# Kernel tuning notes

Measured on AMD Instinct MI355X. Metric: run time of the kernel, lower is better.

## Reference

```python
import jax, jax.numpy as jnp
import numpy as np

B, C, D, H, W = 2, 32, 16, 64, 64
SCALER = 8
CK = C // SCALER  # qk channels = 4


def setup_inputs() -> dict:
    key = jax.random.key(0)
    ks = jax.random.split(key, 8)
    s = 0.05
    return {
        "x": jax.random.normal(ks[0], (B, C, D, H, W), dtype=jnp.float32),
        "Wk": jax.random.normal(ks[1], (CK, C), dtype=jnp.float32) * s,
        "bk": jax.random.normal(ks[2], (CK,), dtype=jnp.float32) * s,
        "Wq": jax.random.normal(ks[3], (CK, C), dtype=jnp.float32) * s,
        "bq": jax.random.normal(ks[4], (CK,), dtype=jnp.float32) * s,
        "Wv": jax.random.normal(ks[5], (C, C), dtype=jnp.float32) * s,
        "bv": jax.random.normal(ks[6], (C,), dtype=jnp.float32) * s,
        "gamma": jnp.ones((1,), dtype=jnp.float32),
    }


def _proj(x, Wt, b):
    # 1x1x1 Conv3d == channel matmul: (o,c) x (b,c,d,h,w) -> (b,o,d,h,w)
    y = jnp.einsum('oc,bcdhw->bodhw', Wt, x) + b[None, :, None, None, None]
    return y


def reference(x, Wk, bk, Wq, bq, Wv, bv, gamma):
    b, c, d, h, w = x.shape
    hw = h * w
    xk = _proj(x, Wk, bk).reshape(b, -1, hw)   # (b, ck*d, hw)
    xq = _proj(x, Wq, bq).reshape(b, -1, hw)   # (b, ck*d, hw)
    xv = _proj(x, Wv, bv).reshape(b, -1, hw)   # (b, c*d,  hw)
    # dot[b,i,j] = sum_e xk[b,e,i] * xq[b,e,j]  -> (b, hw, hw)
    dot = jnp.einsum('bei,bej->bij', xk, xq)
    att = jax.nn.softmax(dot, axis=-1)          # softmax over last dim
    # x_a[b,m,i] = sum_j xv[b,m,j] * att[b,i,j]
    x_a = jnp.einsum('bmj,bij->bmi', xv, att)
    x_a = x_a.reshape(b, c, d, h, w)
    return gamma[0] * x + x_a
```

## Files before the change

kernel.cpp:

```cpp
#include <hip/hip_runtime.h>
#include <hip/hip_bf16.h>

#define B_   2
#define C_   32
#define D_   16
#define HW_  4096
#define CK_  4
#define E_   64
#define M_   512
#define JC_  4

typedef __attribute__((ext_vector_type(8)))  short bf16x8;
typedef __attribute__((ext_vector_type(16))) float f32x16;

union U4 { unsigned int u[4]; bf16x8 v; };

__device__ __forceinline__ short f2bf(float f) {
    __hip_bfloat16 h = __float2bfloat16(f);
    return *reinterpret_cast<short*>(&h);
}
__device__ __forceinline__ unsigned short f2bfu(float f) {
    __hip_bfloat16 h = __float2bfloat16(f);
    return *reinterpret_cast<unsigned short*>(&h);
}

__global__ void prep_kernel(
    const float* __restrict__ Wk, const float* __restrict__ bk,
    const float* __restrict__ Wq, const float* __restrict__ bq,
    const float* __restrict__ Wv, const float* __restrict__ bv,
    short* __restrict__ Wall, float* __restrict__ ball)
{
    int t = threadIdx.x;
    for (int i = t; i < 64*C_; i += 256) {
        int o = i >> 5, cc = i & 31;
        float val = (o < 32) ? Wv[o*C_ + cc]
                  : (o < 36) ? Wk[(o-32)*C_ + cc]
                  : (o < 40) ? Wq[(o-36)*C_ + cc] : 0.f;
        Wall[o*C_ + cc] = f2bf(val);
    }
    if (t < 64)
        ball[t] = (t < 32) ? bv[t] : (t < 36) ? bk[t-32] : (t < 40) ? bq[t-36] : 0.f;
}

__global__ __launch_bounds__(256) void proj_kernel(
    const float* __restrict__ x,
    const short* __restrict__ Wall, const float* __restrict__ ball,
    short* __restrict__ xk, short* __restrict__ xq,
    __hip_bfloat16* __restrict__ v)
{
    __shared__ short s_k[32*16], s_q[32*16];
    const int t    = threadIdx.x;
    const int lane = t & 63;
    const int w    = t >> 6;
    const int h    = lane >> 5;
    const int c    = lane & 31;

    const int pt = blockIdx.x & 127;
    const int dg = (blockIdx.x >> 7) & 3;
    const int b  = blockIdx.x >> 9;
    const int d  = dg*4 + w;
    const int p0 = pt*32;

    bf16x8 af[2][2];
    #pragma unroll
    for (int mt = 0; mt < 2; ++mt)
        #pragma unroll
        for (int s = 0; s < 2; ++s)
            af[mt][s] = *(const bf16x8*)(Wall + (mt*32 + c)*C_ + s*16 + h*8);

    U4 xb[2];
    #pragma unroll
    for (int s = 0; s < 2; ++s) {
        #pragma unroll
        for (int j = 0; j < 4; ++j) {
            int c0 = s*16 + h*8 + 2*j;
            union { float f; unsigned int u; } ua, ub;
            ua.f = x[(((size_t)(b*C_ + c0  )*D_ + d)*HW_) + p0 + c];
            ub.f = x[(((size_t)(b*C_ + c0+1)*D_ + d)*HW_) + p0 + c];
            xb[s].u[j] = __builtin_amdgcn_perm(ub.u, ua.u, 0x07060302);
        }
    }

    f32x16 a0, a1;
    #pragma unroll
    for (int r = 0; r < 16; ++r) { a0[r] = 0.f; a1[r] = 0.f; }
    #pragma unroll
    for (int s = 0; s < 2; ++s) {
        a0 = __builtin_amdgcn_mfma_f32_32x32x16_bf16(af[0][s], xb[s].v, a0, 0, 0, 0);
        a1 = __builtin_amdgcn_mfma_f32_32x32x16_bf16(af[1][s], xb[s].v, a1, 0, 0, 0);
    }

    #pragma unroll
    for (int r = 0; r < 16; ++r) {
        int o = (r & 3) + 8*(r >> 2) + 4*h;
        v[((size_t)b*M_ + (o*D_ + d))*HW_ + p0 + c] = __float2bfloat16(a0[r] + ball[o]);
    }

    #pragma unroll
    for (int r = 0; r < 4; ++r) {
        if (h == 0) s_k[c*16 + w*4 + r] = f2bf(a1[r] + ball[32 + r]);
        else        s_q[c*16 + w*4 + r] = f2bf(a1[r] + ball[36 + r]);
    }
    __syncthreads();

    const int p = t >> 3, seg = t & 7;
    size_t gb = ((size_t)b*HW_ + p0 + p)*E_ + dg*16 + seg*2;
    *(unsigned int*)(xk + gb) = *(const unsigned int*)(&s_k[p*16 + seg*2]);
    *(unsigned int*)(xq + gb) = *(const unsigned int*)(&s_q[p*16 + seg*2]);
}

__device__ __forceinline__ void load_lds16(const short* g, short* l) {
    __builtin_amdgcn_global_load_lds((const __attribute__((address_space(1))) void*)g,
                                     (__attribute__((address_space(3))) void*)l,
                                     16, 0, 0);
}

__global__ __launch_bounds__(256, 2) void attn_kernel(
    const short* __restrict__ xk_, const short* __restrict__ xq_,
    const short* __restrict__ v_,
    unsigned short* __restrict__ Op, float* __restrict__ lw)
{
    __shared__ short s_xq[2][2048];
    __shared__ short s_v [2][4096];

    const int t    = threadIdx.x;
    const int lane = t & 63;
    const int w    = t >> 6;
    const int h    = lane >> 5;
    const int c    = lane & 31;

    const int cls  = blockIdx.x & 7;
    const int b    = cls >> 2, mg = cls & 3;
    const int rest = blockIdx.x >> 3;
    const int ig   = rest & 15;
    const int jc   = rest >> 4;
    const int i0   = ig*256 + w*64;
    const int jbase = jc*(HW_/JC_);

    const short* xk_g = xk_ + (size_t)b*HW_*E_;
    const short* xq_g = xq_ + (size_t)b*HW_*E_;
    const short* v_g  = v_  + (size_t)b*M_*HW_ + (size_t)mg*128*HW_;

    bf16x8 kb[2][4];
    #pragma unroll
    for (int H = 0; H < 2; ++H)
        #pragma unroll
        for (int s = 0; s < 4; ++s)
            kb[H][s] = *(const bf16x8*)(xk_g + (size_t)(i0 + H*32 + c)*E_ + s*16 + h*8);

    f32x16 accA[4], accB[4];
    #pragma unroll
    for (int mt = 0; mt < 4; ++mt)
        #pragma unroll
        for (int r = 0; r < 16; ++r) { accA[mt][r] = 0.f; accB[mt][r] = 0.f; }
    float lpA = 0.f, lpB = 0.f;

    auto stage = [&](int buf, int j0) {
        {
            int r_ = w*8 + (lane>>3), cc = (lane&7) ^ (r_&7);
            load_lds16(xq_g + (size_t)(j0 + r_)*E_ + cc*8, &s_xq[buf][w*512]);
        }
        #pragma unroll
        for (int k = 0; k < 2; ++k) {
            int r0 = w*32 + k*16;
            int r_ = r0 + (lane>>2);
            int g  = (lane&3) ^ ((r_>>1)&3);
            load_lds16(v_g + (size_t)r_*HW_ + j0 + g*8, &s_v[buf][r0*32]);
        }
    };

    stage(0, jbase);
    __syncthreads();

    for (int it = 0; it < (HW_/JC_)/32; ++it) {
        const int cur = it & 1;
        if (it + 1 < (HW_/JC_)/32)
            stage(cur^1, jbase + (it+1)*32);

        f32x16 stA, stB;
        #pragma unroll
        for (int r = 0; r < 16; ++r) { stA[r] = 0.f; stB[r] = 0.f; }
        #pragma unroll
        for (int s = 0; s < 4; ++s) {
            int slot = (s*2 + h) ^ (c & 7);
            bf16x8 a1 = *(const bf16x8*)(&s_xq[cur][c*64 + slot*8]);
            stA = __builtin_amdgcn_mfma_f32_32x32x16_bf16(a1, kb[0][s], stA, 0, 0, 0);
            stB = __builtin_amdgcn_mfma_f32_32x32x16_bf16(a1, kb[1][s], stB, 0, 0, 0);
        }

        unsigned int dqA[8], pdA[8], dqB[8], pdB[8];
        #pragma unroll
        for (int qd = 0; qd < 8; ++qd) {
            union { float f; unsigned int u; } ua, ub;
            float a0 = __expf(stA[2*qd]);
            float a1v = __expf(stA[2*qd+1]);
            lpA += a0 + a1v;
            ua.f = a0; ub.f = a1v;
            dqA[qd] = __builtin_amdgcn_perm(ub.u, ua.u, 0x07060302);
            float b0 = __expf(stB[2*qd]);
            float b1v = __expf(stB[2*qd+1]);
            lpB += b0 + b1v;
            ua.f = b0; ub.f = b1v;
            dqB[qd] = __builtin_amdgcn_perm(ub.u, ua.u, 0x07060302);
        }
        #pragma unroll
        for (int qd = 0; qd < 8; ++qd) {
            pdA[qd] = __shfl_xor(dqA[qd], 32, 64);
            pdB[qd] = __shfl_xor(dqB[qd], 32, 64);
        }

        #pragma unroll
        for (int s2 = 0; s2 < 2; ++s2) {
            U4 a2A, a2B;
            if (s2 == 0) {
                a2A.u[0] = h ? pdA[2] : dqA[0];  a2B.u[0] = h ? pdB[2] : dqB[0];
                a2A.u[1] = h ? pdA[3] : dqA[1];  a2B.u[1] = h ? pdB[3] : dqB[1];
                a2A.u[2] = h ? dqA[2] : pdA[0];  a2B.u[2] = h ? dqB[2] : pdB[0];
                a2A.u[3] = h ? dqA[3] : pdA[1];  a2B.u[3] = h ? dqB[3] : pdB[1];
            } else {
                a2A.u[0] = h ? pdA[6] : dqA[4];  a2B.u[0] = h ? pdB[6] : dqB[4];
                a2A.u[1] = h ? pdA[7] : dqA[5];  a2B.u[1] = h ? pdB[7] : dqB[5];
                a2A.u[2] = h ? dqA[6] : pdA[4];  a2B.u[2] = h ? dqB[6] : pdB[4];
                a2A.u[3] = h ? dqA[7] : pdA[5];  a2B.u[3] = h ? dqB[7] : pdB[5];
            }
            #pragma unroll
            for (int mt = 0; mt < 4; ++mt) {
                int rowm = mt*32 + c;
                int slot = (s2*2 + h) ^ ((rowm>>1)&3);
                bf16x8 vb = *(const bf16x8*)(&s_v[cur][rowm*32 + slot*8]);
                accA[mt] = __builtin_amdgcn_mfma_f32_32x32x16_bf16(a2A.v, vb, accA[mt], 0, 0, 0);
                accB[mt] = __builtin_amdgcn_mfma_f32_32x32x16_bf16(a2B.v, vb, accB[mt], 0, 0, 0);
            }
        }
        __syncthreads();
    }

    float lA = lpA + __shfl_xor(lpA, 32, 64);
    float lB = lpB + __shfl_xor(lpB, 32, 64);
    if (h == 0 && mg == 0) {
        lw[(size_t)(jc*B_ + b)*HW_ + i0 + c]      = lA;
        lw[(size_t)(jc*B_ + b)*HW_ + i0 + 32 + c] = lB;
    }

    const size_t opb = ((size_t)(jc*B_ + b)*M_ + mg*128)*HW_;
    #pragma unroll
    for (int mt = 0; mt < 4; ++mt) {
        size_t rb = opb + (size_t)(mt*32 + c)*HW_ + i0;
        #pragma unroll
        for (int g = 0; g < 4; ++g) {
            ushort4 s4;
            s4.x = f2bfu(accA[mt][4*g+0]);
            s4.y = f2bfu(accA[mt][4*g+1]);
            s4.z = f2bfu(accA[mt][4*g+2]);
            s4.w = f2bfu(accA[mt][4*g+3]);
            *(ushort4*)(Op + rb + 8*g + 4*h) = s4;
            s4.x = f2bfu(accB[mt][4*g+0]);
            s4.y = f2bfu(accB[mt][4*g+1]);
            s4.z = f2bfu(accB[mt][4*g+2]);
            s4.w = f2bfu(accB[mt][4*g+3]);
            *(ushort4*)(Op + rb + 32 + 8*g + 4*h) = s4;
        }
    }
}

__global__ __launch_bounds__(256) void reduce_kernel(
    const float* __restrict__ x, const float* __restrict__ gamma_p,
    const unsigned short* __restrict__ Op, const float* __restrict__ lw,
    float* __restrict__ out)
{
    size_t idx = ((size_t)blockIdx.x*256 + threadIdx.x)*4;
    int i = idx & (HW_-1);
    size_t bm = idx >> 12;
    int m = bm & (M_-1);
    int b = (int)(bm >> 9);

    float4 o = {0.f,0.f,0.f,0.f};
    float4 l = {0.f,0.f,0.f,0.f};
    #pragma unroll
    for (int jc = 0; jc < JC_; ++jc) {
        ushort4 ov = *(const ushort4*)(Op + ((size_t)(jc*B_ + b)*M_ + m)*HW_ + i);
        o.x += __uint_as_float((unsigned int)ov.x << 16);
        o.y += __uint_as_float((unsigned int)ov.y << 16);
        o.z += __uint_as_float((unsigned int)ov.z << 16);
        o.w += __uint_as_float((unsigned int)ov.w << 16);
        float4 lv = *(const float4*)(lw + (size_t)(jc*B_ + b)*HW_ + i);
        l.x += lv.x; l.y += lv.y; l.z += lv.z; l.w += lv.w;
    }
    const float gamma = gamma_p[0];
    float4 xv = *(const float4*)(x + idx);
    float4 r;
    r.x = gamma*xv.x + o.x / l.x;
    r.y = gamma*xv.y + o.y / l.y;
    r.z = gamma*xv.z + o.z / l.z;
    r.w = gamma*xv.w + o.w / l.w;
    *(float4*)(out + idx) = r;
}

extern "C" void kernel_launch(void* const* d_in, const int* in_sizes, int n_in,
                              void* d_out, int out_size, void* d_ws, size_t ws_size,
                              hipStream_t stream)
{
    const float* x     = (const float*)d_in[0];
    const float* Wk    = (const float*)d_in[1];
    const float* bk    = (const float*)d_in[2];
    const float* Wq    = (const float*)d_in[3];
    const float* bq    = (const float*)d_in[4];
    const float* Wv    = (const float*)d_in[5];
    const float* bv    = (const float*)d_in[6];
    const float* gamma = (const float*)d_in[7];
    float* out = (float*)d_out;

    char* ws = (char*)d_ws;
    short*          xk   = (short*)(ws);
    short*          xq   = (short*)(ws + (1<<20));
    short*          v    = (short*)(ws + (2<<20));
    short*          Wall = (short*)(ws + (10<<20));
    float*          ball = (float*)(ws + (10<<20) + 4096);
    unsigned short* Op   = (unsigned short*)(ws + (10<<20) + 8192);
    float*          lw   = (float*)(ws + (10<<20) + 8192
                                    + (size_t)JC_*B_*M_*HW_*2);

    prep_kernel<<<1, 256, 0, stream>>>(Wk, bk, Wq, bq, Wv, bv, Wall, ball);
    proj_kernel<<<B_*(D_/4)*(HW_/32), 256, 0, stream>>>(x, Wall, ball, xk, xq,
                                                        (__hip_bfloat16*)v);
    attn_kernel<<<8*16*JC_, 256, 0, stream>>>(xk, xq, v, Op, lw);
    reduce_kernel<<<(B_*M_*HW_)/(256*4), 256, 0, stream>>>(x, gamma, Op, lw, out);
}
```

Baseline: 161.4 us.

## Halve per-wave query rows, double grid, use permlane32_swap for P transpose

Each wave now handles 32 query rows instead of 64, which halves the accumulator and score registers so the launch bound can request 4 blocks per CU, and the grid doubles to 1024 blocks. The cross-half exchange of the softmax probabilities is done with permlane32_swap instead of shuffles and selects. The cost is that each staged xq/V tile in LDS now feeds half as many MFMAs, so LDS and global traffic per unit of work doubles.

```diff
diff --git a/kernel.cpp b/kernel.cpp
--- a/kernel.cpp
+++ b/kernel.cpp
@@ -12,6 +12,7 @@
 
 typedef __attribute__((ext_vector_type(8)))  short bf16x8;
 typedef __attribute__((ext_vector_type(16))) float f32x16;
+typedef __attribute__((ext_vector_type(2)))  unsigned int u32x2;
 
 union U4 { unsigned int u[4]; bf16x8 v; };
 
@@ -115,7 +116,7 @@
                                      16, 0, 0);
 }
 
-__global__ __launch_bounds__(256, 2) void attn_kernel(
+__global__ __launch_bounds__(256, 4) void attn_kernel(
     const short* __restrict__ xk_, const short* __restrict__ xq_,
     const short* __restrict__ v_,
     unsigned short* __restrict__ Op, float* __restrict__ lw)
@@ -132,28 +133,26 @@
     const int cls  = blockIdx.x & 7;
     const int b    = cls >> 2, mg = cls & 3;
     const int rest = blockIdx.x >> 3;
-    const int ig   = rest & 15;
-    const int jc   = rest >> 4;
-    const int i0   = ig*256 + w*64;
+    const int ig   = rest & 31;
+    const int jc   = rest >> 5;
+    const int i0   = ig*128 + w*32;
     const int jbase = jc*(HW_/JC_);
 
     const short* xk_g = xk_ + (size_t)b*HW_*E_;
     const short* xq_g = xq_ + (size_t)b*HW_*E_;
     const short* v_g  = v_  + (size_t)b*M_*HW_ + (size_t)mg*128*HW_;
 
-    bf16x8 kb[2][4];
-    #pragma unroll
-    for (int H = 0; H < 2; ++H)
-        #pragma unroll
-        for (int s = 0; s < 4; ++s)
-            kb[H][s] = *(const bf16x8*)(xk_g + (size_t)(i0 + H*32 + c)*E_ + s*16 + h*8);
-
-    f32x16 accA[4], accB[4];
+    bf16x8 kb[4];
+    #pragma unroll
+    for (int s = 0; s < 4; ++s)
+        kb[s] = *(const bf16x8*)(xk_g + (size_t)(i0 + c)*E_ + s*16 + h*8);
+
+    f32x16 acc[4];
     #pragma unroll
     for (int mt = 0; mt < 4; ++mt)
         #pragma unroll
-        for (int r = 0; r < 16; ++r) { accA[mt][r] = 0.f; accB[mt][r] = 0.f; }
-    float lpA = 0.f, lpB = 0.f;
+        for (int r = 0; r < 16; ++r) acc[mt][r] = 0.f;
+    float lp = 0.f;
 
     auto stage = [&](int buf, int j0) {
         {
@@ -177,70 +176,55 @@
         if (it + 1 < (HW_/JC_)/32)
             stage(cur^1, jbase + (it+1)*32);
 
-        f32x16 stA, stB;
-        #pragma unroll
-        for (int r = 0; r < 16; ++r) { stA[r] = 0.f; stB[r] = 0.f; }
+        f32x16 st;
+        #pragma unroll
+        for (int r = 0; r < 16; ++r) st[r] = 0.f;
         #pragma unroll
         for (int s = 0; s < 4; ++s) {
             int slot = (s*2 + h) ^ (c & 7);
             bf16x8 a1 = *(const bf16x8*)(&s_xq[cur][c*64 + slot*8]);
-            stA = __builtin_amdgcn_mfma_f32_32x32x16_bf16(a1, kb[0][s], stA, 0, 0, 0);
-            stB = __builtin_amdgcn_mfma_f32_32x32x16_bf16(a1, kb[1][s], stB, 0, 0, 0);
-        }
-
-        unsigned int dqA[8], pdA[8], dqB[8], pdB[8];
+            st = __builtin_amdgcn_mfma_f32_32x32x16_bf16(a1, kb[s], st, 0, 0, 0);
+        }
+
+        unsigned int dq[8];
         #pragma unroll
         for (int qd = 0; qd < 8; ++qd) {
             union { float f; unsigned int u; } ua, ub;
-            float a0 = __expf(stA[2*qd]);
-            float a1v = __expf(stA[2*qd+1]);
-            lpA += a0 + a1v;
-            ua.f = a0; ub.f = a1v;
-            dqA[qd] = __builtin_amdgcn_perm(ub.u, ua.u, 0x07060302);
-            float b0 = __expf(stB[2*qd]);
-            float b1v = __expf(stB[2*qd+1]);
-            lpB += b0 + b1v;
-            ua.f = b0; ub.f = b1v;
-            dqB[qd] = __builtin_amdgcn_perm(ub.u, ua.u, 0x07060302);
-        }
-        #pragma unroll
-        for (int qd = 0; qd < 8; ++qd) {
-            pdA[qd] = __shfl_xor(dqA[qd], 32, 64);
-            pdB[qd] = __shfl_xor(dqB[qd], 32, 64);
+            float e0 = __expf(st[2*qd]);
+            float e1 = __expf(st[2*qd+1]);
+            lp += e0 + e1;
+            ua.f = e0; ub.f = e1;
+            dq[qd] = __builtin_amdgcn_perm(ub.u, ua.u, 0x07060302);
+        }
+
+        U4 a2[2];
+        {
+            u32x2 r02 = __builtin_amdgcn_permlane32_swap(dq[0], dq[2], false, false);
+            u32x2 r13 = __builtin_amdgcn_permlane32_swap(dq[1], dq[3], false, false);
+            u32x2 r46 = __builtin_amdgcn_permlane32_swap(dq[4], dq[6], false, false);
+            u32x2 r57 = __builtin_amdgcn_permlane32_swap(dq[5], dq[7], false, false);
+            a2[0].u[0] = r02[0]; a2[0].u[1] = r13[0];
+            a2[0].u[2] = r02[1]; a2[0].u[3] = r13[1];
+            a2[1].u[0] = r46[0]; a2[1].u[1] = r57[0];
+            a2[1].u[2] = r46[1]; a2[1].u[3] = r57[1];
         }
 
         #pragma unroll
         for (int s2 = 0; s2 < 2; ++s2) {
-            U4 a2A, a2B;
-            if (s2 == 0) {
-                a2A.u[0] = h ? pdA[2] : dqA[0];  a2B.u[0] = h ? pdB[2] : dqB[0];
-                a2A.u[1] = h ? pdA[3] : dqA[1];  a2B.u[1] = h ? pdB[3] : dqB[1];
-                a2A.u[2] = h ? dqA[2] : pdA[0];  a2B.u[2] = h ? dqB[2] : pdB[0];
-                a2A.u[3] = h ? dqA[3] : pdA[1];  a2B.u[3] = h ? dqB[3] : pdB[1];
-            } else {
-                a2A.u[0] = h ? pdA[6] : dqA[4];  a2B.u[0] = h ? pdB[6] : dqB[4];
-                a2A.u[1] = h ? pdA[7] : dqA[5];  a2B.u[1] = h ? pdB[7] : dqB[5];
-                a2A.u[2] = h ? dqA[6] : pdA[4];  a2B.u[2] = h ? dqB[6] : pdB[4];
-                a2A.u[3] = h ? dqA[7] : pdA[5];  a2B.u[3] = h ? dqB[7] : pdB[5];
-            }
             #pragma unroll
             for (int mt = 0; mt < 4; ++mt) {
                 int rowm = mt*32 + c;
                 int slot = (s2*2 + h) ^ ((rowm>>1)&3);
                 bf16x8 vb = *(const bf16x8*)(&s_v[cur][rowm*32 + slot*8]);
-                accA[mt] = __builtin_amdgcn_mfma_f32_32x32x16_bf16(a2A.v, vb, accA[mt], 0, 0, 0);
-                accB[mt] = __builtin_amdgcn_mfma_f32_32x32x16_bf16(a2B.v, vb, accB[mt], 0, 0, 0);
+                acc[mt] = __builtin_amdgcn_mfma_f32_32x32x16_bf16(a2[s2].v, vb, acc[mt], 0, 0, 0);
             }
         }
         __syncthreads();
     }
 
-    float lA = lpA + __shfl_xor(lpA, 32, 64);
-    float lB = lpB + __shfl_xor(lpB, 32, 64);
-    if (h == 0 && mg == 0) {
-        lw[(size_t)(jc*B_ + b)*HW_ + i0 + c]      = lA;
-        lw[(size_t)(jc*B_ + b)*HW_ + i0 + 32 + c] = lB;
-    }
+    float l = lp + __shfl_xor(lp, 32, 64);
+    if (h == 0 && mg == 0)
+        lw[(size_t)(jc*B_ + b)*HW_ + i0 + c] = l;
 
     const size_t opb = ((size_t)(jc*B_ + b)*M_ + mg*128)*HW_;
     #pragma unroll
@@ -249,16 +233,11 @@
         #pragma unroll
         for (int g = 0; g < 4; ++g) {
             ushort4 s4;
-            s4.x = f2bfu(accA[mt][4*g+0]);
-            s4.y = f2bfu(accA[mt][4*g+1]);
-            s4.z = f2bfu(accA[mt][4*g+2]);
-            s4.w = f2bfu(accA[mt][4*g+3]);
+            s4.x = f2bfu(acc[mt][4*g+0]);
+            s4.y = f2bfu(acc[mt][4*g+1]);
+            s4.z = f2bfu(acc[mt][4*g+2]);
+            s4.w = f2bfu(acc[mt][4*g+3]);
             *(ushort4*)(Op + rb + 8*g + 4*h) = s4;
-            s4.x = f2bfu(accB[mt][4*g+0]);
-            s4.y = f2bfu(accB[mt][4*g+1]);
-            s4.z = f2bfu(accB[mt][4*g+2]);
-            s4.w = f2bfu(accB[mt][4*g+3]);
-            *(ushort4*)(Op + rb + 32 + 8*g + 4*h) = s4;
         }
     }
 }
@@ -323,6 +302,6 @@
     prep_kernel<<<1, 256, 0, stream>>>(Wk, bk, Wq, bq, Wv, bv, Wall, ball);
     proj_kernel<<<B_*(D_/4)*(HW_/32), 256, 0, stream>>>(x, Wall, ball, xk, xq,
                                                         (__hip_bfloat16*)v);
-    attn_kernel<<<8*16*JC_, 256, 0, stream>>>(xk, xq, v, Op, lw);
+    attn_kernel<<<8*32*JC_, 256, 0, stream>>>(xk, xq, v, Op, lw);
     reduce_kernel<<<(B_*M_*HW_)/(256*4), 256, 0, stream>>>(x, gamma, Op, lw, out);
 }
```

After: 162.5 us. Within noise of the previous version (+0.7%).
